# Optimization experiments

Hardware: AMD Instinct MI355X
Metric: run time of the kernel (lower is better)

The kernel has to match this reference:

```python
import jax, jax.numpy as jnp
import numpy as np

N_HIDDEN = 512
BATCH = 16
MAX_LEN = 4096


def setup_inputs() -> dict:
    key = jax.random.key(0)
    k1, k2, k3 = jax.random.split(key, 3)
    h = jax.random.normal(k1, (BATCH, N_HIDDEN, MAX_LEN), dtype=jnp.float32)
    # Conv1d weight [out_ch=3*nh, in_ch=nh, kernel=2], fan-in scaled
    W = jax.random.normal(k2, (3 * N_HIDDEN, N_HIDDEN, 2), dtype=jnp.float32) / np.float32(np.sqrt(2.0 * N_HIDDEN))
    b = 0.02 * jax.random.normal(k3, (3 * N_HIDDEN,), dtype=jnp.float32)
    b = b.at[2 * N_HIDDEN:].set(1.0)  # init_gate_bias on the gate third of the bias
    # lengths: grouped (unique_consecutive) and sorted descending, padded into width MAX_LEN
    N = jnp.array([4096] * 4 + [3000] * 4 + [2048] * 4 + [1000] * 4, dtype=jnp.int32)
    return {"h": h, "W": W, "b": b, "N": N}


def _conv_reduce(h, W, b):
    # _reduce: Conv1d(nh -> 3*nh, kernel=2, stride=2) then gated combine (dropout=0).
    B, C, L = h.shape
    Lp = L + (L % 2)
    x = jnp.pad(h, ((0, 0), (0, 0), (0, Lp - L))).reshape(B, C, Lp // 2, 2)
    lrg = jnp.einsum('bclk,ock->bol', x, W) + b[None, :, None]  # [B, 3C, L//2]
    l = lrg[:, :C]
    r = jnp.tanh(lrg[:, C:2 * C])
    g = jax.nn.sigmoid(lrg[:, 2 * C:])
    return l * g + r * (1.0 - g)


def _forward(h, W, b, N):
    B, nh, L = h.shape
    # Nfp2 = largest power of two <= N ; M = 2*(N - Nfp2)
    Nfp2 = (2 ** jnp.floor(jnp.log2(N.astype(jnp.float32)))).astype(N.dtype)
    M = 2 * (N - Nfp2)
    # --- prefix reduce + suffix cat (padded/masked equivalent of _suffix_cat) ---
    # conv is local (k=2, s=2), so reducing the full padded width gives identical
    # values at the kept positions j < M//2.
    red = _conv_reduce(h, W, b)                      # [B, nh, ceil(L/2)]
    red = jnp.pad(red, ((0, 0), (0, 0), (0, L - red.shape[-1])))
    j = jnp.arange(L)
    half = (M // 2)[:, None]                         # [B, 1]
    take_red = j[None, :] < half                     # first M//2 slots <- reduced prefix
    idx = jnp.where(take_red, j[None, :], jnp.minimum(j[None, :] + half, L - 1))
    suf = jnp.take_along_axis(h, jnp.broadcast_to(idx[:, None, :], (B, nh, L)), axis=2)
    cur = jnp.where(take_red[:, None, :], red, suf)  # per-seq length now Nfp2 (power of 2)
    n = Nfp2
    # --- halving tree reduction; freeze sequences that reached length 1 ---
    steps = int(np.floor(np.log2(L)))
    for _ in range(steps):
        red = _conv_reduce(cur, W, b)
        neww = red.shape[-1]
        active = (n > 1)[:, None, None]
        cur = jnp.where(active, red, cur[:, :, :neww])
        n = jnp.where(n > 1, n // 2, n)
    return cur[:, :, 0]  # squeeze(-1) -> [B, nh]


def reference(h, W, b, N):
    return _forward(h, W, b, N)
```

## Files before the change

### kernel.cpp

```cpp
#include <hip/hip_runtime.h>

#define BATCH 16
#define CH 512
#define OC 1536
#define KDIM 1024
#define LMAX 4096
#define WGLOB_SZ 3145728

typedef __attribute__((ext_vector_type(8))) _Float16 h8v;
typedef __attribute__((ext_vector_type(4))) float f4v;

__device__ __forceinline__ int nfp2_of(int n) { return 1 << (31 - __clz(n)); }

__device__ __forceinline__ unsigned short h2u(_Float16 h) {
  union { _Float16 h; unsigned short u; } v; v.h = h; return v.u;
}

__device__ __forceinline__ void layout(const int* __restrict__ Nvec, int b,
                                       size_t& offC0, size_t& offA, size_t& offB,
                                       int& n, int& nfp2, int& half) {
  size_t c0t = 0, at = 0, bt = 0, c0o = 0, ao = 0, bo = 0;
  n = 2; nfp2 = 2; half = 0;
#pragma unroll 1
  for (int i = 0; i < BATCH; ++i) {
    int ni = Nvec[i];
    int f = nfp2_of(ni);
    int hf = ni - f;
    size_t cs = (size_t)((hf + 127) & ~127) << 11;
    size_t as = (size_t)(f >> 1) << 11;
    size_t bs = (size_t)(f >> 2) << 11;
    if (i < b) { c0o += cs; ao += as; bo += bs; }
    if (i == b) { n = ni; nfp2 = f; half = hf; }
    c0t += cs; at += as; bt += bs;
  }
  offC0 = (size_t)WGLOB_SZ + c0o;
  offA = (size_t)WGLOB_SZ + c0t + ao;
  offB = (size_t)WGLOB_SZ + c0t + at + bo;
}

__device__ __forceinline__ void gload16(const void* g, void* l) {
  __builtin_amdgcn_global_load_lds((const __attribute__((address_space(1))) void*)g,
                                   (__attribute__((address_space(3))) void*)l, 16, 0, 0);
}

__global__ __launch_bounds__(256) void prep_w_k(const float* __restrict__ W, char* __restrict__ ws) {
  int idx = blockIdx.x * 256 + threadIdx.x;
  if (idx >= 16 * 1536) return;
  int step = idx / 1536;
  int o = idx - step * 1536;
  const float* src = W + (size_t)o * KDIM + step * 64;
  unsigned short hb[64];
#pragma unroll
  for (int t = 0; t < 64; ++t) hb[t] = h2u((_Float16)src[t]);
  uint4* d4 = (uint4*)(ws + ((size_t)idx << 7));
#pragma unroll
  for (int s = 0; s < 8; ++s) {
    int oc = (s ^ (o & 7)) * 8;
    uint4 v;
    v.x = (unsigned)hb[oc + 0] | ((unsigned)hb[oc + 1] << 16);
    v.y = (unsigned)hb[oc + 2] | ((unsigned)hb[oc + 3] << 16);
    v.z = (unsigned)hb[oc + 4] | ((unsigned)hb[oc + 5] << 16);
    v.w = (unsigned)hb[oc + 6] | ((unsigned)hb[oc + 7] << 16);
    d4[s] = v;
  }
}

__global__ __launch_bounds__(256) void reorg_h_k(const float* __restrict__ h,
                                                 const int* __restrict__ Nvec,
                                                 char* __restrict__ ws,
                                                 float* __restrict__ dout, int mode) {
  __shared__ char T[32 * 256];
  const int b = blockIdx.z;
  size_t offC0, offA, offB; int n, nfp2, half;
  layout(Nvec, b, offC0, offA, offB, n, nfp2, half);
  const int tid = threadIdx.x;
  const int by = blockIdx.y;
  const int c0 = by * 64;

  if (mode == 1 && nfp2 == 1) {
    if (blockIdx.x == 0 && tid < 64)
      dout[(size_t)b * CH + c0 + tid] = h[(size_t)b * CH * LMAX + (size_t)(c0 + tid) * LMAX];
    return;
  }

  const int d0 = blockIdx.x * 32;
  int dlo, dhi, soff;
  size_t base;
  if (mode == 0) { dlo = 0; dhi = half; soff = 0; base = offC0; }
  else { dlo = half >> 1; dhi = nfp2 >> 1; soff = half; base = offA; }
  if (d0 >= dhi || d0 + 32 <= dlo) return;

  const float* hb = h + (size_t)b * CH * LMAX;

#pragma unroll
  for (int q = 0; q < 8; ++q) {
    int id = q * 256 + tid;
    int cl = id >> 5;
    int dl = id & 31;
    int d = d0 + dl;
    bool ok = (d < dhi) && (d >= dlo);
    float2 v;
    v.x = 0.f; v.y = 0.f;
    if (ok) v = *(const float2*)(hb + (size_t)(c0 + cl) * LMAX + 2 * d + soff);
    unsigned u = (unsigned)h2u((_Float16)v.x) | ((unsigned)h2u((_Float16)v.y) << 16);
    int g = cl >> 2;
    *(unsigned*)(T + dl * 256 + ((g ^ (dl & 15)) << 4) + (cl & 3) * 4) = u;
  }
  __syncthreads();
#pragma unroll
  for (int qq = 0; qq < 2; ++qq) {
    int gid = qq * 256 + tid;
    int dl = gid >> 4;
    int s = gid & 15;
    int d = d0 + dl;
    if (d >= dhi || d < dlo) continue;
    uint4 val = *(const uint4*)(T + dl * 256 + ((s ^ (dl & 15)) << 4));
    size_t dst = base + ((size_t)d << 11) + (size_t)((2 * by + (s >> 3)) << 7) +
                 (((s & 7) ^ (d & 7)) << 4);
    *(uint4*)(ws + dst) = val;
  }
}

__global__ __launch_bounds__(512, 2) void mfma_level_k(const float* __restrict__ bias,
                                                       const int* __restrict__ Nvec,
                                                       char* __restrict__ ws,
                                                       float* __restrict__ dout,
                                                       int level, int tiles) {
  __shared__ char smem[114688];
  const int id = blockIdx.x;
  const int o0 = (id & 7) * 64;
  const int r2 = id >> 3;
  const int xb = r2 % tiles;
  const int b = r2 / tiles;
  if (b >= BATCH) return;

  size_t offC0, offA, offB; int n, nfp2, half;
  layout(Nvec, b, offC0, offA, offB, n, nfp2, half);

  int cols;
  size_t inOff, outOff;
  if (level == 0) {
    if (half == 0) return;
    cols = half;
    inOff = offC0;
    outOff = offA;
  } else {
    int w = nfp2 >> (level - 1);
    if (w < 2) return;
    cols = w >> 1;
    inOff = (level & 1) ? offA : offB;
    outOff = (level & 1) ? offB : offA;
  }
  const bool fin = (level > 0) && ((nfp2 >> level) == 1);
  const int l0 = xb * 256;
  if (l0 >= cols) return;

  const int tid = threadIdx.x;
  const int lane = tid & 63, wid = tid >> 6;
  const int lane15 = lane & 15, lq = lane >> 4;
  const int rg = wid & 1, cg = wid >> 1;
  const char* inp = ws + inOff;

  unsigned aoff[3]; int adst[3];
#pragma unroll
  for (int q = 0; q < 3; ++q) {
    int d = q * 8192 + tid * 16;
    int r = d >> 7;
    int p = d & 127;
    int o = ((r >> 6) << 9) + o0 + (r & 63);
    aoff[q] = ((unsigned)o << 7) + p;
    adst[q] = q * 8192 + wid * 1024;
  }
  unsigned boff[4]; int bdst[4];
#pragma unroll
  for (int q = 0; q < 4; ++q) {
    int d = q * 8192 + tid * 16;
    int l = d >> 7;
    int p = d & 127;
    int lc = l0 + l; if (lc > cols - 1) lc = cols - 1;
    boff[q] = ((unsigned)lc << 11) + p;
    bdst[q] = q * 8192 + wid * 1024;
  }

#define STAGE(st, sel) do {                                                  \
    char* Ab = smem + (sel) * 57344;                                         \
    char* Bb = Ab + 24576;                                                   \
    unsigned ka = (unsigned)(st) * 196608u;                                  \
    unsigned kb = (unsigned)(st) << 7;                                       \
    _Pragma("unroll") for (int q = 0; q < 3; ++q)                            \
      gload16(ws + ka + aoff[q], Ab + adst[q]);                              \
    _Pragma("unroll") for (int q = 0; q < 4; ++q)                            \
      gload16(inp + kb + boff[q], Bb + bdst[q]);                             \
  } while (0)

  f4v acc[6][4];
#pragma unroll
  for (int m = 0; m < 6; ++m)
#pragma unroll
    for (int cf = 0; cf < 4; ++cf) acc[m][cf] = (f4v){0.f, 0.f, 0.f, 0.f};

  STAGE(0, 0);
  __syncthreads();

#pragma unroll 1
  for (int st = 0; st < 16; ++st) {
    const int cur = st & 1;
    if (st + 1 < 16) STAGE(st + 1, cur ^ 1);
    const char* Asb = smem + cur * 57344;
    const char* Bsb = Asb + 24576;

#pragma unroll
    for (int s2 = 0; s2 < 2; ++s2) {
      const int oct = (s2 << 2) | lq;
      h8v bh[4];
#pragma unroll
      for (int cf = 0; cf < 4; ++cf) {
        int ll = cg * 64 + cf * 16 + lane15;
        bh[cf] = *(const h8v*)(Bsb + ll * 128 + ((oct ^ (ll & 7)) << 4));
      }
#pragma unroll
      for (int m = 0; m < 6; ++m) {
        int rr = (m >> 1) * 64 + rg * 32 + (m & 1) * 16 + lane15;
        h8v ah = *(const h8v*)(Asb + rr * 128 + ((oct ^ (rr & 7)) << 4));
#pragma unroll
        for (int cf = 0; cf < 4; ++cf)
          acc[m][cf] = __builtin_amdgcn_mfma_f32_16x16x32_f16(ah, bh[cf], acc[m][cf], 0, 0, 0);
      }
    }
    __syncthreads();
  }
#undef STAGE

  char* outp = ws + outOff;
#pragma unroll
  for (int s = 0; s < 2; ++s) {
#pragma unroll
    for (int cf = 0; cf < 4; ++cf) {
      f4v vl = acc[s][cf], vr = acc[2 + s][cf], vg = acc[4 + s][cf];
      int l = l0 + cg * 64 + cf * 16 + lane15;
      if (l >= cols) continue;
      int P = l >> 1, par = l & 1;
#pragma unroll
      for (int j = 0; j < 4; ++j) {
        int c = o0 + rg * 32 + s * 16 + lq * 4 + j;
        float zl = vl[j] + bias[c];
        float zr = vr[j] + bias[CH + c];
        float zg = vg[j] + bias[2 * CH + c];
        float g = 1.f / (1.f + __expf(-zg));
        float rt = 1.f - 2.f / (1.f + __expf(2.f * zr));
        float val = zl * g + rt * (1.f - g);
        if (fin) {
          if (l == 0) dout[(size_t)b * CH + c] = val;
        } else {
          int k = 2 * c + par;
          size_t byte = ((size_t)P << 11) + (size_t)((k >> 6) << 7) +
                        ((((k >> 3) & 7) ^ (P & 7)) << 4) + ((k & 7) << 1);
          *(unsigned short*)(outp + byte) = h2u((_Float16)val);
        }
      }
    }
  }
}

extern "C" void kernel_launch(void* const* d_in, const int* in_sizes, int n_in,
                              void* d_out, int out_size, void* d_ws, size_t ws_size,
                              hipStream_t stream) {
  const float* h = (const float*)d_in[0];
  const float* W = (const float*)d_in[1];
  const float* bias = (const float*)d_in[2];
  const int* Nvec = (const int*)d_in[3];
  float* dout = (float*)d_out;
  char* ws = (char*)d_ws;

  prep_w_k<<<dim3(96), 256, 0, stream>>>(W, ws);
  reorg_h_k<<<dim3(64, 8, BATCH), 256, 0, stream>>>(h, Nvec, ws, dout, 0);
  reorg_h_k<<<dim3(64, 8, BATCH), 256, 0, stream>>>(h, Nvec, ws, dout, 1);

  mfma_level_k<<<dim3(4 * 8 * BATCH), 512, 0, stream>>>(bias, Nvec, ws, dout, 0, 4);
  for (int lev = 1; lev <= 12; ++lev) {
    int colsmax = LMAX >> lev;
    int tiles = (colsmax + 255) / 256; if (tiles < 1) tiles = 1;
    mfma_level_k<<<dim3(tiles * 8 * BATCH), 512, 0, stream>>>(bias, Nvec, ws, dout, lev, tiles);
  }
}
```

Measured before the change: 542.1 us.

## Deepen MFMA GEMM pipeline with triple-buffered B and one barrier per step

Splits the shared-memory staging into a double-buffered A (weight) tile and a triple-buffered B (activation) tile. B is prefetched two stages ahead, and the global-to-LDS copies are issued in the middle of each k-step, after the fragment reads. Each iteration now uses one explicit s_waitcnt vmcnt plus a barrier instead of two __syncthreads, and the MFMA block is wrapped in s_setprio to favour the math wave. The goal is to hide global load latency behind MFMA work. In exchange it uses more LDS and relies on hand-counted vmcnt values being correct.

```diff
diff --git a/kernel.cpp b/kernel.cpp
--- a/kernel.cpp
+++ b/kernel.cpp
@@ -126,7 +126,7 @@
                                                        char* __restrict__ ws,
                                                        float* __restrict__ dout,
                                                        int level, int tiles) {
-  __shared__ char smem[114688];
+  __shared__ char smem[147456];
   const int id = blockIdx.x;
   const int o0 = (id & 7) * 64;
   const int r2 = id >> 3;
@@ -182,13 +182,15 @@
     bdst[q] = q * 8192 + wid * 1024;
   }
 
-#define STAGE(st, sel) do {                                                  \
-    char* Ab = smem + (sel) * 57344;                                         \
-    char* Bb = Ab + 24576;                                                   \
+#define STAGE_A(st, sel) do {                                                \
+    char* Ab = smem + (sel) * 24576;                                         \
     unsigned ka = (unsigned)(st) * 196608u;                                  \
-    unsigned kb = (unsigned)(st) << 7;                                       \
     _Pragma("unroll") for (int q = 0; q < 3; ++q)                            \
       gload16(ws + ka + aoff[q], Ab + adst[q]);                              \
+  } while (0)
+#define STAGE_B(st, sel) do {                                                \
+    char* Bb = smem + 49152 + (sel) * 32768;                                 \
+    unsigned kb = (unsigned)(st) << 7;                                       \
     _Pragma("unroll") for (int q = 0; q < 4; ++q)                            \
       gload16(inp + kb + boff[q], Bb + bdst[q]);                             \
   } while (0)
@@ -199,15 +201,21 @@
 #pragma unroll
     for (int cf = 0; cf < 4; ++cf) acc[m][cf] = (f4v){0.f, 0.f, 0.f, 0.f};
 
-  STAGE(0, 0);
-  __syncthreads();
-
+  STAGE_A(0, 0);
+  STAGE_B(0, 0);
+  STAGE_B(1, 1);
+
+  int rb = 0;
+  int wb = 2;
 #pragma unroll 1
   for (int st = 0; st < 16; ++st) {
-    const int cur = st & 1;
-    if (st + 1 < 16) STAGE(st + 1, cur ^ 1);
-    const char* Asb = smem + cur * 57344;
-    const char* Bsb = Asb + 24576;
+    if (st < 15) asm volatile("s_waitcnt vmcnt(4) lgkmcnt(0)" ::: "memory");
+    else         asm volatile("s_waitcnt vmcnt(0) lgkmcnt(0)" ::: "memory");
+    __builtin_amdgcn_s_barrier();
+    asm volatile("" ::: "memory");
+
+    const char* Asb = smem + (st & 1) * 24576;
+    const char* Bsb = smem + 49152 + rb * 32768;
 
 #pragma unroll
     for (int s2 = 0; s2 < 2; ++s2) {
@@ -218,18 +226,27 @@
         int ll = cg * 64 + cf * 16 + lane15;
         bh[cf] = *(const h8v*)(Bsb + ll * 128 + ((oct ^ (ll & 7)) << 4));
       }
+      h8v ah[6];
 #pragma unroll
       for (int m = 0; m < 6; ++m) {
         int rr = (m >> 1) * 64 + rg * 32 + (m & 1) * 16 + lane15;
-        h8v ah = *(const h8v*)(Asb + rr * 128 + ((oct ^ (rr & 7)) << 4));
+        ah[m] = *(const h8v*)(Asb + rr * 128 + ((oct ^ (rr & 7)) << 4));
+      }
+      if (s2 == 0) { if (st + 1 < 16) STAGE_A(st + 1, (st + 1) & 1); }
+      else         { if (st + 2 < 16) STAGE_B(st + 2, wb); }
+      __builtin_amdgcn_s_setprio(1);
+#pragma unroll
+      for (int m = 0; m < 6; ++m)
 #pragma unroll
         for (int cf = 0; cf < 4; ++cf)
-          acc[m][cf] = __builtin_amdgcn_mfma_f32_16x16x32_f16(ah, bh[cf], acc[m][cf], 0, 0, 0);
-      }
+          acc[m][cf] = __builtin_amdgcn_mfma_f32_16x16x32_f16(ah[m], bh[cf], acc[m][cf], 0, 0, 0);
+      __builtin_amdgcn_s_setprio(0);
     }
-    __syncthreads();
-  }
-#undef STAGE
+    rb = (rb == 2) ? 0 : rb + 1;
+    wb = (wb == 2) ? 0 : wb + 1;
+  }
+#undef STAGE_A
+#undef STAGE_B
 
   char* outp = ws + outOff;
 #pragma unroll
```

After: 531.9 us. Within noise of the previous version (-1.9%).
